# Kernel optimization log

Measured on AMD Instinct MI355X. Metric: run time of the kernel, lower is better.

Reference implementation:

```python
import jax, jax.numpy as jnp
import numpy as np
from jax import lax

# dims: batch, seq, d_model, d_inner, d_state, dt_rank, conv_k, fno_modes, n_inner_blocks, d_model_out
B_, L_, D_, DI_, N_, R_, K_, M_, NB_, DOUT_ = 2, 256, 256, 512, 32, 16, 4, 16, 7, 76416
EPS = 1e-5


def setup_inputs() -> dict:
    key = jax.random.key(0)
    ks = iter(jax.random.split(key, 48))
    nrm = lambda shape, s=0.02: jax.random.normal(next(ks), shape, jnp.float32) * s
    a_log = jnp.log(jnp.arange(1, N_ + 1, dtype=jnp.float32))  # Mamba S4D-real init
    return {
        "x": jax.random.normal(next(ks), (B_, L_, D_), jnp.float32),
        "ln_w": jnp.ones((NB_, D_), jnp.float32), "ln_b": jnp.zeros((NB_, D_), jnp.float32),
        "in_w": nrm((NB_, 2 * DI_, D_)),
        "conv_w": nrm((NB_, DI_, K_)), "conv_b": jnp.zeros((NB_, DI_), jnp.float32),
        "xproj_w": nrm((NB_, R_ + N_, DI_)),
        "dt_w": nrm((NB_, DI_, R_)), "dt_b": jnp.full((NB_, DI_), -4.0, jnp.float32),
        "A_log": jnp.broadcast_to(a_log, (NB_, DI_, N_)),
        "Cmat": nrm((NB_, DI_, N_)), "Dvec": jnp.ones((NB_, DI_), jnp.float32),
        "spec_r": nrm((NB_, DI_, M_)), "spec_i": nrm((NB_, DI_, M_)),
        "out_w": nrm((NB_, D_, DI_)),
        "fln_w": jnp.ones((D_,), jnp.float32), "fln_b": jnp.zeros((D_,), jnp.float32),
        "f_in_w": nrm((2 * DI_, D_)),
        "f_conv_w": nrm((DI_, K_)), "f_conv_b": jnp.zeros((DI_,), jnp.float32),
        "f_xproj_w": nrm((R_ + N_, DI_)),
        "f_dt_w": nrm((DI_, R_)), "f_dt_b": jnp.full((DI_,), -4.0, jnp.float32),
        "f_A_log": jnp.broadcast_to(a_log, (DI_, N_)),
        "f_Cmat": nrm((DI_, N_)), "f_Dvec": jnp.ones((DI_,), jnp.float32),
        "f_spec_r": nrm((DI_, M_)), "f_spec_i": nrm((DI_, M_)),
        "f_out_w": nrm((DOUT_, DI_)),
    }


def _silu(v):
    return v * jax.nn.sigmoid(v)


def _layernorm(v, w, b):
    mu = v.mean(-1, keepdims=True)
    var = ((v - mu) ** 2).mean(-1, keepdims=True)
    return (v - mu) * lax.rsqrt(var + EPS) * w + b


def _mixer(h, in_w, conv_w, conv_b, xproj_w, dt_w, dt_b, A_log, Cmat, Dvec, spec_r, spec_i, out_w):
    # MambawithfixedC_time: selective scan with learned fixed C + 1D FNO spectral branch
    B, L, _ = h.shape
    Di, K = conv_w.shape
    R = dt_w.shape[1]
    x, z = jnp.split(h @ in_w.T, 2, axis=-1)                      # (B,L,Di) each
    # causal depthwise conv along sequence
    xc = jnp.pad(x.transpose(0, 2, 1), ((0, 0), (0, 0), (K - 1, 0)))  # (B,Di,L+K-1)
    x = lax.conv_general_dilated(xc, conv_w[:, None, :], (1,), 'VALID',
                                 feature_group_count=Di)          # (B,Di,L)
    x = _silu(x.transpose(0, 2, 1) + conv_b)                      # (B,L,Di)
    dbl = x @ xproj_w.T                                           # (B,L,R+N)
    dt = jax.nn.softplus(dbl[..., :R] @ dt_w.T + dt_b)            # (B,L,Di)
    Bmat = dbl[..., R:]                                           # (B,L,N)
    A = -jnp.exp(A_log)                                           # (Di,N)
    dA = jnp.exp(dt[..., None] * A)                               # (B,L,Di,N)
    dBx = dt[..., None] * Bmat[:, :, None, :] * x[..., None]      # (B,L,Di,N)

    def step(hstate, inputs):
        a_t, bx_t = inputs
        hstate = a_t * hstate + bx_t
        return hstate, jnp.einsum('bdn,dn->bd', hstate, Cmat)

    h0 = jnp.zeros((B, Di, A.shape[1]), x.dtype)
    _, y = lax.scan(step, h0, (dA.transpose(1, 0, 2, 3), dBx.transpose(1, 0, 2, 3)))
    y = y.transpose(1, 0, 2) + Dvec * x                           # (B,L,Di)
    # FNO spectral branch: keep first M rFFT modes over sequence axis
    M = spec_r.shape[1]
    Xf = jnp.fft.rfft(x, axis=1)[:, :M, :]                        # (B,M,Di) complex
    W = (spec_r + 1j * spec_i).T                                  # (M,Di)
    y = y + jnp.fft.irfft(Xf * W, n=L, axis=1)
    return (y * _silu(z)) @ out_w.T


def reference(x, ln_w, ln_b, in_w, conv_w, conv_b, xproj_w, dt_w, dt_b, A_log, Cmat,
              Dvec, spec_r, spec_i, out_w, fln_w, fln_b, f_in_w, f_conv_w, f_conv_b,
              f_xproj_w, f_dt_w, f_dt_b, f_A_log, f_Cmat, f_Dvec, f_spec_r, f_spec_i,
              f_out_w):
    hidden, residual = x, None
    for i in range(ln_w.shape[0]):  # inner Blocks (prenorm residual + mixer)
        residual = hidden if residual is None else residual + hidden
        hidden = _layernorm(residual, ln_w[i], ln_b[i])
        hidden = _mixer(hidden, in_w[i], conv_w[i], conv_b[i], xproj_w[i], dt_w[i],
                        dt_b[i], A_log[i], Cmat[i], Dvec[i], spec_r[i], spec_i[i], out_w[i])
    # finalBlock: residual add + norm + mixer projecting to d_model_out
    residual = residual + hidden
    hidden = _layernorm(residual, fln_w, fln_b)
    return _mixer(hidden, f_in_w, f_conv_w, f_conv_b, f_xproj_w, f_dt_w, f_dt_b,
                  f_A_log, f_Cmat, f_Dvec, f_spec_r, f_spec_i, f_out_w)
```

## Files before the change

### kernel.cpp

```cpp
#include <hip/hip_runtime.h>
#include <hip/hip_bf16.h>

#define BLr 512
#define Dm 256
#define DIc 512
#define DOUTc 76416

typedef short bf16x8 __attribute__((ext_vector_type(8)));
typedef float f32x16 __attribute__((ext_vector_type(16)));

__device__ __forceinline__ unsigned short f2bf(float f){
  unsigned u = __builtin_bit_cast(unsigned, f);
  u += 0x7FFFu + ((u >> 16) & 1u);
  return (unsigned short)(u >> 16);
}

__device__ __forceinline__ void gl_lds16(const void* g, void* l){
  __builtin_amdgcn_global_load_lds(
      (const __attribute__((address_space(1))) unsigned int*)g,
      (__attribute__((address_space(3))) unsigned int*)l, 16, 0, 0);
}

__device__ __forceinline__ bf16x8 cvt8(float4 a, float4 b){
  unsigned q0 = (unsigned)f2bf(a.x) | ((unsigned)f2bf(a.y) << 16);
  unsigned q1 = (unsigned)f2bf(a.z) | ((unsigned)f2bf(a.w) << 16);
  unsigned q2 = (unsigned)f2bf(b.x) | ((unsigned)f2bf(b.y) << 16);
  unsigned q3 = (unsigned)f2bf(b.z) | ((unsigned)f2bf(b.w) << 16);
  uint4 u{q0, q1, q2, q3};
  return __builtin_bit_cast(bf16x8, u);
}

__global__ __launch_bounds__(256) void ln_inproj_kernel(
    float* __restrict__ xz, const float* __restrict__ src,
    const float* __restrict__ lw, const float* __restrict__ lb,
    const float* __restrict__ iw)
{
  __shared__ __align__(16) float Aln[32][260];
  __shared__ __align__(16) float Wf[64*256];
  const int tid = threadIdx.x;
  const int m0 = blockIdx.y*32, n0 = blockIdx.x*64;
  const int wv = tid>>6, lane = tid&63;
  #pragma unroll
  for (int i = 0; i < 16; ++i){
    int col = i*4 + wv;
    int sc  = lane ^ (col&7);
    gl_lds16(iw + (size_t)(n0+col)*256 + sc*4, (void*)((char*)Wf + col*1024));
  }
  float4 w4 = *(const float4*)(lw + lane*4);
  float4 b4 = *(const float4*)(lb + lane*4);
  #pragma unroll
  for (int rr = 0; rr < 8; ++rr){
    int row = wv*8 + rr;
    float4 v = *(const float4*)(src + (m0+row)*Dm + lane*4);
    float s  = v.x+v.y+v.z+v.w;
    float s2 = v.x*v.x+v.y*v.y+v.z*v.z+v.w*v.w;
    #pragma unroll
    for (int m = 1; m < 64; m <<= 1){ s += __shfl_xor(s,m); s2 += __shfl_xor(s2,m); }
    float mu = s*(1.f/256.f), var = s2*(1.f/256.f) - mu*mu;
    float rs = rsqrtf(var + 1e-5f);
    float4 o;
    o.x = (v.x-mu)*rs*w4.x + b4.x;
    o.y = (v.y-mu)*rs*w4.y + b4.y;
    o.z = (v.z-mu)*rs*w4.z + b4.z;
    o.w = (v.w-mu)*rs*w4.w + b4.w;
    *(float4*)&Aln[row][lane*4] = o;
  }
  __syncthreads();
  const int ty = tid>>4, tx = tid&15;
  float acc[2][4] = {{0,0,0,0},{0,0,0,0}};
  #pragma unroll 4
  for (int kk = 0; kk < 64; ++kk){
    float4 a0 = *(const float4*)&Aln[ty][kk*4];
    float4 a1 = *(const float4*)&Aln[ty+16][kk*4];
    #pragma unroll
    for (int j = 0; j < 4; ++j){
      int col = tx + 16*j;
      float4 w = *(const float4*)&Wf[(col*64 + (kk ^ (col&7)))*4];
      acc[0][j] += a0.x*w.x + a0.y*w.y + a0.z*w.z + a0.w*w.w;
      acc[1][j] += a1.x*w.x + a1.y*w.y + a1.z*w.z + a1.w*w.w;
    }
  }
  #pragma unroll
  for (int j = 0; j < 4; ++j){
    xz[(m0+ty)*1024    + n0 + tx + 16*j] = acc[0][j];
    xz[(m0+ty+16)*1024 + n0 + tx + 16*j] = acc[1][j];
  }
}

__global__ __launch_bounds__(256) void conv_xproj_dt_kernel(
    float* __restrict__ xc, float* __restrict__ dbl, float* __restrict__ dtv,
    const float* __restrict__ xz, const float* __restrict__ cw,
    const float* __restrict__ cb, const float* __restrict__ xw,
    const float* __restrict__ dw, const float* __restrict__ db)
{
  __shared__ __align__(16) float xcr[512];
  __shared__ float dblq[16];
  const int row = blockIdx.x, tid = threadIdx.x;
  const int t = row & 255;
  #pragma unroll
  for (int h = 0; h < 2; ++h){
    int d = tid + h*256;
    float4 w = *(const float4*)(cw + d*4);
    float acc = cb[d];
    const float* xp = xz + (size_t)row*1024 + d;
    if (t >= 3) acc += w.x*xp[-3072] + w.y*xp[-2048] + w.z*xp[-1024] + w.w*xp[0];
    else {
      acc += w.w*xp[0];
      if (t >= 1) acc += w.z*xp[-1024];
      if (t >= 2) acc += w.y*xp[-2048];
    }
    float v = acc / (1.f + __expf(-acc));
    xcr[d] = v;
    xc[row*DIc + d] = v;
  }
  __syncthreads();
  const int wv = tid>>6, lane = tid&63;
  float4 xa = *(const float4*)&xcr[lane*4];
  float4 xb = *(const float4*)&xcr[256 + lane*4];
  #pragma unroll
  for (int o = 0; o < 12; ++o){
    int oo = wv*12 + o;
    const float* wr = xw + oo*DIc;
    float4 wa = *(const float4*)(wr + lane*4);
    float4 wb = *(const float4*)(wr + 256 + lane*4);
    float p = xa.x*wa.x + xa.y*wa.y + xa.z*wa.z + xa.w*wa.w
            + xb.x*wb.x + xb.y*wb.y + xb.z*wb.z + xb.w*wb.w;
    #pragma unroll
    for (int m = 1; m < 64; m <<= 1) p += __shfl_xor(p, m);
    if (lane == 0){
      dbl[row*48 + oo] = p;
      if (oo < 16) dblq[oo] = p;
    }
  }
  __syncthreads();
  #pragma unroll
  for (int h = 0; h < 2; ++h){
    int d = tid + h*256;
    const float4* wr = (const float4*)(dw + d*16);
    float4 w0 = wr[0], w1 = wr[1], w2 = wr[2], w3 = wr[3];
    float acc = db[d];
    acc += dblq[0]*w0.x  + dblq[1]*w0.y  + dblq[2]*w0.z  + dblq[3]*w0.w;
    acc += dblq[4]*w1.x  + dblq[5]*w1.y  + dblq[6]*w1.z  + dblq[7]*w1.w;
    acc += dblq[8]*w2.x  + dblq[9]*w2.y  + dblq[10]*w2.z + dblq[11]*w2.w;
    acc += dblq[12]*w3.x + dblq[13]*w3.y + dblq[14]*w3.z + dblq[15]*w3.w;
    dtv[row*DIc + d] = (acc > 20.f) ? acc : log1pf(__expf(acc));
  }
}

__global__ __launch_bounds__(256) void scan_fft_gate_kernel(
    float* __restrict__ g, unsigned short* __restrict__ gbf,
    const float* __restrict__ xc, const float* __restrict__ dtv,
    const float* __restrict__ dbl, const float* __restrict__ xz,
    const float* __restrict__ A_log, const float* __restrict__ Cmat,
    const float* __restrict__ Dvec, const float* __restrict__ sr,
    const float* __restrict__ si)
{
  __shared__ float xs[4][260], dts[4][260], ys[4][260];
  __shared__ float ct[256], st[256];
  __shared__ float Ysr[4][17], Ysi[4][17];
  __shared__ float Pl[2][2][32][65];
  const int tid = threadIdx.x;
  const int b = blockIdx.y, d0 = blockIdx.x*4;
  {
    float sv, cv;
    __sincosf((float)tid * 0.02454369260617026f, &sv, &cv);
    ct[tid] = cv; st[tid] = sv;
  }
  const int dd = tid & 3, tq = tid >> 2;
  #pragma unroll
  for (int i = 0; i < 4; ++i){
    int t = i*64 + tq;
    xs[dd][t]  = xc [(b*256+t)*DIc + d0+dd];
    dts[dd][t] = dtv[(b*256+t)*DIc + d0+dd];
  }
  __syncthreads();
  const int wv = tid>>6, lane = tid&63;
  if (wv < 2){
    const int ch2 = lane>>5;
    const int ddw = wv*2 + ch2;
    const int d = d0 + ddw;
    const int n = lane & 31;
    const int tloc = lane & 31;
    const float A  = -__expf(A_log[d*32+n]);
    const float Cv = Cmat[d*32+n];
    const float* Bp = dbl + (size_t)(b*256)*48 + 16 + n;
    float h = 0.f;
    for (int pass = 0; pass < 4; ++pass){
      #pragma unroll 8
      for (int i = 0; i < 64; ++i){
        int t = pass*64 + i;
        float dtl = dts[ddw][t];
        float xv  = xs[ddw][t];
        float Bv  = Bp[t*48];
        h = __expf(dtl*A)*h + dtl*Bv*xv;
        Pl[wv][ch2][n][i] = h*Cv;
      }
      float s0 = 0.f, s1 = 0.f;
      #pragma unroll 8
      for (int n2 = 0; n2 < 32; ++n2){
        s0 += Pl[wv][ch2][n2][tloc];
        s1 += Pl[wv][ch2][n2][32+tloc];
      }
      ys[ddw][pass*64 + tloc]      = s0;
      ys[ddw][pass*64 + 32 + tloc] = s1;
    }
  } else {
    const int ddw = (wv-2)*2 + (lane>>5);
    const int m = lane & 15, im = (lane>>4) & 1;
    float acc = 0.f;
    for (int t = 0; t < 256; ++t){
      int idx = (m*t) & 255;
      acc += xs[ddw][t] * (im ? st[idx] : ct[idx]);
    }
    float other = __shfl_xor(acc, 16);
    const int d = d0 + ddw;
    float wr = sr[d*16+m], wi = si[d*16+m];
    if (im == 0){
      float Xr = acc, Xi = -other;
      Ysr[ddw][m] = Xr*wr - Xi*wi;
    } else {
      float Xi = -acc, Xr = other;
      Ysi[ddw][m] = Xr*wi + Xi*wr;
    }
  }
  __syncthreads();
  {
    const float Dv = Dvec[d0+dd];
    float yr[16], yi[16];
    #pragma unroll
    for (int m = 0; m < 16; ++m){ yr[m] = Ysr[dd][m]; yi[m] = Ysi[dd][m]; }
    #pragma unroll 2
    for (int i = 0; i < 4; ++i){
      int t = i*64 + tq;
      float fv = 0.5f * yr[0];
      #pragma unroll
      for (int m = 1; m < 16; ++m){
        int idx = (m*t) & 255;
        fv += yr[m]*ct[idx] - yi[m]*st[idx];
      }
      float yv = ys[dd][t] + Dv*xs[dd][t] + fv*0.0078125f;
      float z = xz[(b*256+t)*1024 + 512 + d0+dd];
      float gv = yv * (z / (1.f + __expf(-z)));
      int oi = (b*256+t)*DIc + d0+dd;
      g[oi] = gv;
      gbf[oi] = f2bf(gv);
    }
  }
}

__global__ __launch_bounds__(256) void outproj_resid_kernel(
    float* __restrict__ resid, const float* __restrict__ base,
    const float* __restrict__ g, const float* __restrict__ ow)
{
  __shared__ __align__(16) float Ws2[16*512];
  __shared__ __align__(16) float As[32*128];
  const int tid = threadIdx.x;
  const int wv = tid>>6, lane = tid&63;
  const int n0 = blockIdx.x*16, m0 = blockIdx.y*32;
  const int ty = tid>>4, tx = tid&15;
  #pragma unroll
  for (int i = 0; i < 4; ++i){
    int row = wv*4 + i;
    #pragma unroll
    for (int h = 0; h < 2; ++h){
      int c = h*64 + lane;
      int s = c ^ (row&7);
      gl_lds16(ow + (size_t)(n0+row)*DIc + s*4,
               (void*)((char*)Ws2 + row*2048 + h*1024));
    }
  }
  float b0 = base[(m0+ty)*Dm + n0+tx];
  float b1 = base[(m0+ty+16)*Dm + n0+tx];
  float a00 = 0.f, a10 = 0.f;
  for (int kc = 0; kc < 512; kc += 128){
    if (kc) __syncthreads();
    #pragma unroll
    for (int j = 0; j < 4; ++j){
      int R = wv*8 + j*2;
      int r = R + (lane>>5);
      int c = lane&31;
      int s = c ^ (r&7);
      gl_lds16(g + (size_t)(m0+r)*DIc + kc + s*4,
               (void*)((char*)As + R*512));
    }
    __syncthreads();
    const int kb = kc>>2;
    #pragma unroll
    for (int kk = 0; kk < 32; ++kk){
      float4 a0 = *(const float4*)((const char*)As + ty*512      + ((kk ^ (ty&7))<<4));
      float4 a1 = *(const float4*)((const char*)As + (ty+16)*512 + ((kk ^ (ty&7))<<4));
      float4 w0 = *(const float4*)((const char*)Ws2 + tx*2048 + (((kb+kk) ^ (tx&7))<<4));
      a00 += a0.x*w0.x + a0.y*w0.y + a0.z*w0.z + a0.w*w0.w;
      a10 += a1.x*w0.x + a1.y*w0.y + a1.z*w0.z + a1.w*w0.w;
    }
  }
  resid[(m0+ty)*Dm    + n0+tx] = b0 + a00;
  resid[(m0+ty+16)*Dm + n0+tx] = b1 + a10;
}

__global__ __launch_bounds__(512) void gemm_final2_kernel(
    float* __restrict__ Out, const unsigned short* __restrict__ Gb,
    const float* __restrict__ W)
{
  __shared__ __align__(16) unsigned short As[32768];
  __shared__ __align__(16) unsigned short Wb[4096];
  const int tid = threadIdx.x;
  const int wv = tid>>6, lane = tid&63;
  const int half = lane>>5, lm = lane&31;
  const int nq = wv & 1, mq = wv >> 1;
  const int col = blockIdx.x*64 + nq*32 + lm;
  const int wcol = tid>>3, wkq = tid&7;
  const float* Wsrc = W + (size_t)(blockIdx.x*64 + wcol)*512 + wkq*8;
  unsigned short* Wdst = Wb + (wcol*8 + (wkq ^ (wcol&7)))*8;
  f32x16 acc[4];
  #pragma unroll
  for (int i = 0; i < 4; ++i)
    #pragma unroll
    for (int rg = 0; rg < 16; ++rg) acc[i][rg] = 0.f;

  for (int k0 = 0; k0 < 512; k0 += 64){
    float4 wf0 = *(const float4*)(Wsrc + k0);
    float4 wf1 = *(const float4*)(Wsrc + k0 + 4);
    #pragma unroll
    for (int p = 0; p < 8; ++p){
      int R  = p*64 + wv*8;
      int rr = R + (lane>>3);
      int cg = (lane&7) ^ (rr&7);
      gl_lds16(Gb + rr*512 + k0 + cg*8, (void*)((char*)As + R*128));
    }
    *(bf16x8*)Wdst = cvt8(wf0, wf1);
    __syncthreads();
    #pragma unroll
    for (int j = 0; j < 4; ++j){
      const int c = j*2 + half;
      bf16x8 bv = *(const bf16x8*)(Wb + (((nq*32+lm)*8) + (c ^ ((nq*32+lm)&7)))*8);
      #pragma unroll
      for (int mt = 0; mt < 4; ++mt){
        int rr = mq*128 + mt*32 + lm;
        bf16x8 av = *(const bf16x8*)((const char*)As + (rr*8 + (c ^ (rr&7)))*16);
        acc[mt] = __builtin_amdgcn_mfma_f32_32x32x16_bf16(av, bv, acc[mt], 0, 0, 0);
      }
    }
    __syncthreads();
  }
  #pragma unroll
  for (int mt = 0; mt < 4; ++mt){
    int rbase = mq*128 + mt*32 + 4*half;
    #pragma unroll
    for (int rg = 0; rg < 16; ++rg){
      int row = rbase + (rg&3) + 8*(rg>>2);
      Out[(size_t)row*DOUTc + col] = acc[mt][rg];
    }
  }
}

extern "C" void kernel_launch(void* const* d_in, const int* in_sizes, int n_in,
                              void* d_out, int out_size, void* d_ws, size_t ws_size,
                              hipStream_t stream)
{
  (void)in_sizes; (void)n_in; (void)out_size; (void)ws_size;
  const float* x       = (const float*)d_in[0];
  const float* ln_w    = (const float*)d_in[1];
  const float* ln_b    = (const float*)d_in[2];
  const float* in_w    = (const float*)d_in[3];
  const float* conv_w  = (const float*)d_in[4];
  const float* conv_b  = (const float*)d_in[5];
  const float* xproj_w = (const float*)d_in[6];
  const float* dt_w    = (const float*)d_in[7];
  const float* dt_b    = (const float*)d_in[8];
  const float* A_log   = (const float*)d_in[9];
  const float* Cmat    = (const float*)d_in[10];
  const float* Dvec    = (const float*)d_in[11];
  const float* spec_r  = (const float*)d_in[12];
  const float* spec_i  = (const float*)d_in[13];
  const float* out_w   = (const float*)d_in[14];
  const float* fln_w   = (const float*)d_in[15];
  const float* fln_b   = (const float*)d_in[16];
  const float* f_in_w  = (const float*)d_in[17];
  const float* f_conv_w= (const float*)d_in[18];
  const float* f_conv_b= (const float*)d_in[19];
  const float* f_xproj = (const float*)d_in[20];
  const float* f_dt_w  = (const float*)d_in[21];
  const float* f_dt_b  = (const float*)d_in[22];
  const float* f_A_log = (const float*)d_in[23];
  const float* f_Cmat  = (const float*)d_in[24];
  const float* f_Dvec  = (const float*)d_in[25];
  const float* f_spec_r= (const float*)d_in[26];
  const float* f_spec_i= (const float*)d_in[27];
  const float* f_out_w = (const float*)d_in[28];

  float* ws   = (float*)d_ws;
  float* resid = ws;
  float* xz    = ws + 131072;
  float* xcb   = ws + 655360;
  float* dblb  = ws + 917504;
  float* dtb   = ws + 942080;
  float* gb    = ws + 1204224;
  unsigned short* g_bf = (unsigned short*)(ws + 1466368);
  float* outp = (float*)d_out;

  for (int i = 0; i < 8; ++i){
    const bool fin = (i == 7);
    const float* lw = fin ? fln_w   : ln_w    + i*256;
    const float* lb = fin ? fln_b   : ln_b    + i*256;
    const float* iw = fin ? f_in_w  : in_w    + i*262144;
    const float* cw = fin ? f_conv_w: conv_w  + i*2048;
    const float* cb = fin ? f_conv_b: conv_b  + i*512;
    const float* xw = fin ? f_xproj : xproj_w + i*24576;
    const float* dw = fin ? f_dt_w  : dt_w    + i*8192;
    const float* db = fin ? f_dt_b  : dt_b    + i*512;
    const float* al = fin ? f_A_log : A_log   + i*16384;
    const float* cm = fin ? f_Cmat  : Cmat    + i*16384;
    const float* dv = fin ? f_Dvec  : Dvec    + i*512;
    const float* sr = fin ? f_spec_r: spec_r  + i*8192;
    const float* si = fin ? f_spec_i: spec_i  + i*8192;

    const float* src = (i == 0) ? x : resid;
    ln_inproj_kernel<<<dim3(16, 16), 256, 0, stream>>>(xz, src, lw, lb, iw);
    conv_xproj_dt_kernel<<<512, 256, 0, stream>>>(xcb, dblb, dtb, xz, cw, cb, xw, dw, db);
    scan_fft_gate_kernel<<<dim3(128, 2), 256, 0, stream>>>(gb, g_bf, xcb, dtb, dblb, xz,
                                                           al, cm, dv, sr, si);
    if (!fin){
      outproj_resid_kernel<<<dim3(16, 16), 256, 0, stream>>>(resid, (i == 0) ? x : resid,
                                                             gb, out_w + i*131072);
    } else {
      gemm_final2_kernel<<<DOUTc/64, 512, 0, stream>>>(outp, g_bf, f_out_w);
    }
  }
}
```

Baseline: 844.9 us.

## Fuse all mixer stages into one persistent kernel with grid barriers

Replaces the per-block sequence of four kernel launches with a single persistent 256-block kernel. Stages (LN+in-proj, conv+xproj+dt, scan+FFT+gate, out-proj+residual) are separated by a software grid barrier built on atomic counters. The aim is to remove launch overhead and inter-kernel gaps across the eight blocks. The trade-off is barrier spin cost and reliance on all 256 blocks being co-resident. The barrier also has a spin timeout that could silently break ordering. The old multi-launch path remains as a fallback when the workspace is too small, and the final large GEMM stays a separate launch.

```diff
diff --git a/kernel.cpp b/kernel.cpp
--- a/kernel.cpp
+++ b/kernel.cpp
@@ -28,6 +28,345 @@
   unsigned q3 = (unsigned)f2bf(b.z) | ((unsigned)f2bf(b.w) << 16);
   uint4 u{q0, q1, q2, q3};
   return __builtin_bit_cast(bf16x8, u);
+}
+
+__device__ __forceinline__ void gsync(unsigned* cnt, unsigned* gen, unsigned nb){
+  __syncthreads();
+  if (threadIdx.x == 0){
+    __threadfence();
+    unsigned g = __hip_atomic_load(gen, __ATOMIC_ACQUIRE, __HIP_MEMORY_SCOPE_AGENT);
+    unsigned a = __hip_atomic_fetch_add(cnt, 1u, __ATOMIC_ACQ_REL, __HIP_MEMORY_SCOPE_AGENT);
+    if (a == nb - 1u){
+      __hip_atomic_store(cnt, 0u, __ATOMIC_RELAXED, __HIP_MEMORY_SCOPE_AGENT);
+      __hip_atomic_fetch_add(gen, 1u, __ATOMIC_RELEASE, __HIP_MEMORY_SCOPE_AGENT);
+    } else {
+      int it = 0;
+      while (__hip_atomic_load(gen, __ATOMIC_ACQUIRE, __HIP_MEMORY_SCOPE_AGENT) == g){
+        __builtin_amdgcn_s_sleep(8);
+        if (++it > 16384) break;
+      }
+    }
+    __threadfence();
+  }
+  __syncthreads();
+}
+
+struct MegaArgs {
+  const float *x, *ln_w, *ln_b, *in_w, *conv_w, *conv_b, *xproj_w, *dt_w, *dt_b,
+              *A_log, *Cmat, *Dvec, *spec_r, *spec_i, *out_w,
+              *fln_w, *fln_b, *f_in_w, *f_conv_w, *f_conv_b, *f_xproj,
+              *f_dt_w, *f_dt_b, *f_A_log, *f_Cmat, *f_Dvec, *f_spec_r, *f_spec_i;
+  float *resid, *xz, *xc, *dbl, *dtv, *g;
+  unsigned short* gbf;
+  unsigned *cnt, *gen;
+};
+
+__global__ __launch_bounds__(256) void mega_kernel(MegaArgs a)
+{
+  __shared__ __align__(16) unsigned char SMEM[98816];
+  const int tid = threadIdx.x;
+  const int blk = blockIdx.x;
+  const int wv = tid>>6, lane = tid&63;
+
+  for (int i = 0; i < 8; ++i){
+    const bool fin = (i == 7);
+    const float* lw  = fin ? a.fln_w   : a.ln_w    + i*256;
+    const float* lb  = fin ? a.fln_b   : a.ln_b    + i*256;
+    const float* iw  = fin ? a.f_in_w  : a.in_w    + i*262144;
+    const float* cw  = fin ? a.f_conv_w: a.conv_w  + i*2048;
+    const float* cb  = fin ? a.f_conv_b: a.conv_b  + i*512;
+    const float* xw  = fin ? a.f_xproj : a.xproj_w + i*24576;
+    const float* dwp = fin ? a.f_dt_w  : a.dt_w    + i*8192;
+    const float* dbp = fin ? a.f_dt_b  : a.dt_b    + i*512;
+    const float* al  = fin ? a.f_A_log : a.A_log   + i*16384;
+    const float* cm  = fin ? a.f_Cmat  : a.Cmat    + i*16384;
+    const float* dv  = fin ? a.f_Dvec  : a.Dvec    + i*512;
+    const float* srp = fin ? a.f_spec_r: a.spec_r  + i*8192;
+    const float* sip = fin ? a.f_spec_i: a.spec_i  + i*8192;
+    const float* src = (i == 0) ? a.x : a.resid;
+
+    {
+      float (*Aln)[260] = (float(*)[260])SMEM;
+      float* Wf = (float*)(SMEM + 33280);
+      const int m0 = (blk>>4)*32, n0 = (blk&15)*64;
+      #pragma unroll
+      for (int q = 0; q < 16; ++q){
+        int col = q*4 + wv;
+        int sc  = lane ^ (col&7);
+        gl_lds16(iw + (size_t)(n0+col)*256 + sc*4, (void*)((char*)Wf + col*1024));
+      }
+      float4 w4 = *(const float4*)(lw + lane*4);
+      float4 b4 = *(const float4*)(lb + lane*4);
+      #pragma unroll
+      for (int rr = 0; rr < 8; ++rr){
+        int row = wv*8 + rr;
+        float4 v = *(const float4*)(src + (size_t)(m0+row)*Dm + lane*4);
+        float s  = v.x+v.y+v.z+v.w;
+        float s2 = v.x*v.x+v.y*v.y+v.z*v.z+v.w*v.w;
+        #pragma unroll
+        for (int m = 1; m < 64; m <<= 1){ s += __shfl_xor(s,m); s2 += __shfl_xor(s2,m); }
+        float mu = s*(1.f/256.f), var = s2*(1.f/256.f) - mu*mu;
+        float rs = rsqrtf(var + 1e-5f);
+        float4 o;
+        o.x = (v.x-mu)*rs*w4.x + b4.x;
+        o.y = (v.y-mu)*rs*w4.y + b4.y;
+        o.z = (v.z-mu)*rs*w4.z + b4.z;
+        o.w = (v.w-mu)*rs*w4.w + b4.w;
+        *(float4*)&Aln[row][lane*4] = o;
+      }
+      __syncthreads();
+      const int ty = tid>>4, tx = tid&15;
+      float acc[2][4] = {{0,0,0,0},{0,0,0,0}};
+      #pragma unroll 4
+      for (int kk = 0; kk < 64; ++kk){
+        float4 a0 = *(const float4*)&Aln[ty][kk*4];
+        float4 a1 = *(const float4*)&Aln[ty+16][kk*4];
+        #pragma unroll
+        for (int j = 0; j < 4; ++j){
+          int col = tx + 16*j;
+          float4 w = *(const float4*)&Wf[(col*64 + (kk ^ (col&7)))*4];
+          acc[0][j] += a0.x*w.x + a0.y*w.y + a0.z*w.z + a0.w*w.w;
+          acc[1][j] += a1.x*w.x + a1.y*w.y + a1.z*w.z + a1.w*w.w;
+        }
+      }
+      #pragma unroll
+      for (int j = 0; j < 4; ++j){
+        a.xz[(size_t)(m0+ty)*1024    + n0 + tx + 16*j] = acc[0][j];
+        a.xz[(size_t)(m0+ty+16)*1024 + n0 + tx + 16*j] = acc[1][j];
+      }
+    }
+    gsync(a.cnt, a.gen, 256);
+
+    {
+      float* xcr  = (float*)SMEM;
+      float* dblq = (float*)(SMEM + 4096);
+      const int r0 = blk*2, r1 = r0 + 1;
+      const int t0 = r0 & 255, t1 = r1 & 255;
+      #pragma unroll
+      for (int h = 0; h < 2; ++h){
+        int d = tid + h*256;
+        float4 w = *(const float4*)(cw + d*4);
+        float cbd = cb[d];
+        {
+          float acc = cbd;
+          const float* xp = a.xz + (size_t)r0*1024 + d;
+          if (t0 >= 3) acc += w.x*xp[-3072] + w.y*xp[-2048] + w.z*xp[-1024] + w.w*xp[0];
+          else {
+            acc += w.w*xp[0];
+            if (t0 >= 1) acc += w.z*xp[-1024];
+            if (t0 >= 2) acc += w.y*xp[-2048];
+          }
+          float v = acc / (1.f + __expf(-acc));
+          xcr[d] = v;
+          a.xc[(size_t)r0*DIc + d] = v;
+        }
+        {
+          float acc = cbd;
+          const float* xp = a.xz + (size_t)r1*1024 + d;
+          if (t1 >= 3) acc += w.x*xp[-3072] + w.y*xp[-2048] + w.z*xp[-1024] + w.w*xp[0];
+          else {
+            acc += w.w*xp[0];
+            if (t1 >= 1) acc += w.z*xp[-1024];
+            if (t1 >= 2) acc += w.y*xp[-2048];
+          }
+          float v = acc / (1.f + __expf(-acc));
+          xcr[512+d] = v;
+          a.xc[(size_t)r1*DIc + d] = v;
+        }
+      }
+      __syncthreads();
+      float4 xa0 = *(const float4*)&xcr[lane*4];
+      float4 xb0 = *(const float4*)&xcr[256 + lane*4];
+      float4 xa1 = *(const float4*)&xcr[512 + lane*4];
+      float4 xb1 = *(const float4*)&xcr[768 + lane*4];
+      #pragma unroll
+      for (int o = 0; o < 12; ++o){
+        int oo = wv*12 + o;
+        const float* wr = xw + oo*DIc;
+        float4 wa = *(const float4*)(wr + lane*4);
+        float4 wb = *(const float4*)(wr + 256 + lane*4);
+        float p0 = xa0.x*wa.x + xa0.y*wa.y + xa0.z*wa.z + xa0.w*wa.w
+                 + xb0.x*wb.x + xb0.y*wb.y + xb0.z*wb.z + xb0.w*wb.w;
+        float p1 = xa1.x*wa.x + xa1.y*wa.y + xa1.z*wa.z + xa1.w*wa.w
+                 + xb1.x*wb.x + xb1.y*wb.y + xb1.z*wb.z + xb1.w*wb.w;
+        #pragma unroll
+        for (int m = 1; m < 64; m <<= 1){ p0 += __shfl_xor(p0, m); p1 += __shfl_xor(p1, m); }
+        if (lane == 0){
+          a.dbl[r0*48 + oo] = p0;
+          a.dbl[r1*48 + oo] = p1;
+          if (oo < 16){ dblq[oo] = p0; dblq[16+oo] = p1; }
+        }
+      }
+      __syncthreads();
+      #pragma unroll
+      for (int h = 0; h < 2; ++h){
+        int d = tid + h*256;
+        const float4* wr4 = (const float4*)(dwp + d*16);
+        float4 w0 = wr4[0], w1 = wr4[1], w2 = wr4[2], w3 = wr4[3];
+        float dbv = dbp[d];
+        float acc0 = dbv;
+        acc0 += dblq[0]*w0.x  + dblq[1]*w0.y  + dblq[2]*w0.z  + dblq[3]*w0.w;
+        acc0 += dblq[4]*w1.x  + dblq[5]*w1.y  + dblq[6]*w1.z  + dblq[7]*w1.w;
+        acc0 += dblq[8]*w2.x  + dblq[9]*w2.y  + dblq[10]*w2.z + dblq[11]*w2.w;
+        acc0 += dblq[12]*w3.x + dblq[13]*w3.y + dblq[14]*w3.z + dblq[15]*w3.w;
+        float acc1 = dbv;
+        acc1 += dblq[16]*w0.x + dblq[17]*w0.y + dblq[18]*w0.z + dblq[19]*w0.w;
+        acc1 += dblq[20]*w1.x + dblq[21]*w1.y + dblq[22]*w1.z + dblq[23]*w1.w;
+        acc1 += dblq[24]*w2.x + dblq[25]*w2.y + dblq[26]*w2.z + dblq[27]*w2.w;
+        acc1 += dblq[28]*w3.x + dblq[29]*w3.y + dblq[30]*w3.z + dblq[31]*w3.w;
+        a.dtv[(size_t)r0*DIc + d] = (acc0 > 20.f) ? acc0 : log1pf(__expf(acc0));
+        a.dtv[(size_t)r1*DIc + d] = (acc1 > 20.f) ? acc1 : log1pf(__expf(acc1));
+      }
+    }
+    gsync(a.cnt, a.gen, 256);
+
+    {
+      float (*xs)[260]  = (float(*)[260])(SMEM);
+      float (*dts)[260] = (float(*)[260])(SMEM + 4160);
+      float (*ys)[260]  = (float(*)[260])(SMEM + 8320);
+      float* ct = (float*)(SMEM + 12480);
+      float* st = (float*)(SMEM + 13504);
+      float (*Ysr)[17] = (float(*)[17])(SMEM + 14528);
+      float (*Ysi)[17] = (float(*)[17])(SMEM + 14800);
+      float (*Pl)[2][32][65] = (float(*)[2][32][65])(SMEM + 15072);
+      const int b = blk>>7, d0 = (blk&127)*4;
+      {
+        float sv, cv;
+        __sincosf((float)tid * 0.02454369260617026f, &sv, &cv);
+        ct[tid] = cv; st[tid] = sv;
+      }
+      const int dd = tid & 3, tq = tid >> 2;
+      #pragma unroll
+      for (int q = 0; q < 4; ++q){
+        int t = q*64 + tq;
+        xs[dd][t]  = a.xc [((size_t)b*256+t)*DIc + d0+dd];
+        dts[dd][t] = a.dtv[((size_t)b*256+t)*DIc + d0+dd];
+      }
+      __syncthreads();
+      if (wv < 2){
+        const int ch2 = lane>>5;
+        const int ddw = wv*2 + ch2;
+        const int d = d0 + ddw;
+        const int n = lane & 31;
+        const int tloc = lane & 31;
+        const float A  = -__expf(al[d*32+n]);
+        const float Cv = cm[d*32+n];
+        const float* Bp = a.dbl + (size_t)(b*256)*48 + 16 + n;
+        float h = 0.f;
+        for (int pass = 0; pass < 4; ++pass){
+          #pragma unroll 8
+          for (int q = 0; q < 64; ++q){
+            int t = pass*64 + q;
+            float dtl = dts[ddw][t];
+            float xv  = xs[ddw][t];
+            float Bv  = Bp[t*48];
+            h = __expf(dtl*A)*h + dtl*Bv*xv;
+            Pl[wv][ch2][n][q] = h*Cv;
+          }
+          float s0 = 0.f, s1 = 0.f;
+          #pragma unroll 8
+          for (int n2 = 0; n2 < 32; ++n2){
+            s0 += Pl[wv][ch2][n2][tloc];
+            s1 += Pl[wv][ch2][n2][32+tloc];
+          }
+          ys[ddw][pass*64 + tloc]      = s0;
+          ys[ddw][pass*64 + 32 + tloc] = s1;
+        }
+      } else {
+        const int ddw = (wv-2)*2 + (lane>>5);
+        const int m = lane & 15, im = (lane>>4) & 1;
+        float acc = 0.f;
+        for (int t = 0; t < 256; ++t){
+          int idx = (m*t) & 255;
+          acc += xs[ddw][t] * (im ? st[idx] : ct[idx]);
+        }
+        float other = __shfl_xor(acc, 16);
+        const int d = d0 + ddw;
+        float wr = srp[d*16+m], wi = sip[d*16+m];
+        if (im == 0){
+          float Xr = acc, Xi = -other;
+          Ysr[ddw][m] = Xr*wr - Xi*wi;
+        } else {
+          float Xi = -acc, Xr = other;
+          Ysi[ddw][m] = Xr*wi + Xi*wr;
+        }
+      }
+      __syncthreads();
+      {
+        const float Dv = dv[d0+dd];
+        float yr[16], yi[16];
+        #pragma unroll
+        for (int m = 0; m < 16; ++m){ yr[m] = Ysr[dd][m]; yi[m] = Ysi[dd][m]; }
+        #pragma unroll 2
+        for (int q = 0; q < 4; ++q){
+          int t = q*64 + tq;
+          float fv = 0.5f * yr[0];
+          #pragma unroll
+          for (int m = 1; m < 16; ++m){
+            int idx = (m*t) & 255;
+            fv += yr[m]*ct[idx] - yi[m]*st[idx];
+          }
+          float yv = ys[dd][t] + Dv*xs[dd][t] + fv*0.0078125f;
+          float z = a.xz[((size_t)b*256+t)*1024 + 512 + d0+dd];
+          float gv = yv * (z / (1.f + __expf(-z)));
+          size_t oi = ((size_t)b*256+t)*DIc + d0+dd;
+          a.g[oi] = gv;
+          a.gbf[oi] = f2bf(gv);
+        }
+      }
+    }
+
+    if (!fin){
+      gsync(a.cnt, a.gen, 256);
+      {
+        float* Ws2 = (float*)SMEM;
+        float* As  = (float*)(SMEM + 32768);
+        const int n0 = (blk&15)*16, m0 = (blk>>4)*32;
+        const int ty = tid>>4, tx = tid&15;
+        const float* base = (i == 0) ? a.x : a.resid;
+        const float* ow = a.out_w + i*131072;
+        #pragma unroll
+        for (int q = 0; q < 4; ++q){
+          int row = wv*4 + q;
+          #pragma unroll
+          for (int h = 0; h < 2; ++h){
+            int c = h*64 + lane;
+            int s = c ^ (row&7);
+            gl_lds16(ow + (size_t)(n0+row)*DIc + s*4,
+                     (void*)((char*)Ws2 + row*2048 + h*1024));
+          }
+        }
+        float b0 = base[(m0+ty)*Dm + n0+tx];
+        float b1 = base[(m0+ty+16)*Dm + n0+tx];
+        float a00 = 0.f, a10 = 0.f;
+        for (int kc = 0; kc < 512; kc += 128){
+          if (kc) __syncthreads();
+          #pragma unroll
+          for (int j = 0; j < 4; ++j){
+            int R = wv*8 + j*2;
+            int r = R + (lane>>5);
+            int c = lane&31;
+            int s = c ^ (r&7);
+            gl_lds16(a.g + (size_t)(m0+r)*DIc + kc + s*4,
+                     (void*)((char*)As + R*512));
+          }
+          __syncthreads();
+          const int kb = kc>>2;
+          #pragma unroll
+          for (int kk = 0; kk < 32; ++kk){
+            float4 a0 = *(const float4*)((const char*)As + ty*512      + ((kk ^ (ty&7))<<4));
+            float4 a1 = *(const float4*)((const char*)As + (ty+16)*512 + ((kk ^ (ty&7))<<4));
+            float4 w0 = *(const float4*)((const char*)Ws2 + tx*2048 + (((kb+kk) ^ (tx&7))<<4));
+            a00 += a0.x*w0.x + a0.y*w0.y + a0.z*w0.z + a0.w*w0.w;
+            a10 += a1.x*w0.x + a1.y*w0.y + a1.z*w0.z + a1.w*w0.w;
+          }
+        }
+        a.resid[(m0+ty)*Dm    + n0+tx] = b0 + a00;
+        a.resid[(m0+ty+16)*Dm + n0+tx] = b1 + a10;
+      }
+      gsync(a.cnt, a.gen, 256);
+    }
+  }
 }
 
 __global__ __launch_bounds__(256) void ln_inproj_kernel(
@@ -51,7 +390,7 @@
   #pragma unroll
   for (int rr = 0; rr < 8; ++rr){
     int row = wv*8 + rr;
-    float4 v = *(const float4*)(src + (m0+row)*Dm + lane*4);
+    float4 v = *(const float4*)(src + (size_t)(m0+row)*Dm + lane*4);
     float s  = v.x+v.y+v.z+v.w;
     float s2 = v.x*v.x+v.y*v.y+v.z*v.z+v.w*v.w;
     #pragma unroll
@@ -358,7 +697,7 @@
                               void* d_out, int out_size, void* d_ws, size_t ws_size,
                               hipStream_t stream)
 {
-  (void)in_sizes; (void)n_in; (void)out_size; (void)ws_size;
+  (void)in_sizes; (void)n_in; (void)out_size;
   const float* x       = (const float*)d_in[0];
   const float* ln_w    = (const float*)d_in[1];
   const float* ln_b    = (const float*)d_in[2];
@@ -397,34 +736,54 @@
   float* dtb   = ws + 942080;
   float* gb    = ws + 1204224;
   unsigned short* g_bf = (unsigned short*)(ws + 1466368);
+  unsigned* barrier_words = (unsigned*)(ws + 1597440);
   float* outp = (float*)d_out;
 
-  for (int i = 0; i < 8; ++i){
-    const bool fin = (i == 7);
-    const float* lw = fin ? fln_w   : ln_w    + i*256;
-    const float* lb = fin ? fln_b   : ln_b    + i*256;
-    const float* iw = fin ? f_in_w  : in_w    + i*262144;
-    const float* cw = fin ? f_conv_w: conv_w  + i*2048;
-    const float* cb = fin ? f_conv_b: conv_b  + i*512;
-    const float* xw = fin ? f_xproj : xproj_w + i*24576;
-    const float* dw = fin ? f_dt_w  : dt_w    + i*8192;
-    const float* db = fin ? f_dt_b  : dt_b    + i*512;
-    const float* al = fin ? f_A_log : A_log   + i*16384;
-    const float* cm = fin ? f_Cmat  : Cmat    + i*16384;
-    const float* dv = fin ? f_Dvec  : Dvec    + i*512;
-    const float* sr = fin ? f_spec_r: spec_r  + i*8192;
-    const float* si = fin ? f_spec_i: spec_i  + i*8192;
-
-    const float* src = (i == 0) ? x : resid;
-    ln_inproj_kernel<<<dim3(16, 16), 256, 0, stream>>>(xz, src, lw, lb, iw);
-    conv_xproj_dt_kernel<<<512, 256, 0, stream>>>(xcb, dblb, dtb, xz, cw, cb, xw, dw, db);
-    scan_fft_gate_kernel<<<dim3(128, 2), 256, 0, stream>>>(gb, g_bf, xcb, dtb, dblb, xz,
-                                                           al, cm, dv, sr, si);
-    if (!fin){
-      outproj_resid_kernel<<<dim3(16, 16), 256, 0, stream>>>(resid, (i == 0) ? x : resid,
-                                                             gb, out_w + i*131072);
-    } else {
-      gemm_final2_kernel<<<DOUTc/64, 512, 0, stream>>>(outp, g_bf, f_out_w);
-    }
-  }
-}
+  const bool mega_ok = ws_size >= (size_t)1597440*4 + 8;
+
+  if (mega_ok){
+    hipMemsetAsync(barrier_words, 0, 8, stream);
+    MegaArgs margs;
+    margs.x = x;       margs.ln_w = ln_w;     margs.ln_b = ln_b;
+    margs.in_w = in_w; margs.conv_w = conv_w; margs.conv_b = conv_b;
+    margs.xproj_w = xproj_w; margs.dt_w = dt_w; margs.dt_b = dt_b;
+    margs.A_log = A_log; margs.Cmat = Cmat; margs.Dvec = Dvec;
+    margs.spec_r = spec_r; margs.spec_i = spec_i; margs.out_w = out_w;
+    margs.fln_w = fln_w; margs.fln_b = fln_b; margs.f_in_w = f_in_w;
+    margs.f_conv_w = f_conv_w; margs.f_conv_b = f_conv_b; margs.f_xproj = f_xproj;
+    margs.f_dt_w = f_dt_w; margs.f_dt_b = f_dt_b; margs.f_A_log = f_A_log;
+    margs.f_Cmat = f_Cmat; margs.f_Dvec = f_Dvec; margs.f_spec_r = f_spec_r;
+    margs.f_spec_i = f_spec_i;
+    margs.resid = resid; margs.xz = xz; margs.xc = xcb; margs.dbl = dblb;
+    margs.dtv = dtb; margs.g = gb; margs.gbf = g_bf;
+    margs.cnt = barrier_words; margs.gen = barrier_words + 1;
+    mega_kernel<<<256, 256, 0, stream>>>(margs);
+  } else {
+    for (int i = 0; i < 8; ++i){
+      const bool fin = (i == 7);
+      const float* lw = fin ? fln_w   : ln_w    + i*256;
+      const float* lb = fin ? fln_b   : ln_b    + i*256;
+      const float* iw = fin ? f_in_w  : in_w    + i*262144;
+      const float* cw = fin ? f_conv_w: conv_w  + i*2048;
+      const float* cb = fin ? f_conv_b: conv_b  + i*512;
+      const float* xw = fin ? f_xproj : xproj_w + i*24576;
+      const float* dw = fin ? f_dt_w  : dt_w    + i*8192;
+      const float* db = fin ? f_dt_b  : dt_b    + i*512;
+      const float* al = fin ? f_A_log : A_log   + i*16384;
+      const float* cm = fin ? f_Cmat  : Cmat    + i*16384;
+      const float* dv = fin ? f_Dvec  : Dvec    + i*512;
+      const float* sr = fin ? f_spec_r: spec_r  + i*8192;
+      const float* si = fin ? f_spec_i: spec_i  + i*8192;
+      const float* src = (i == 0) ? x : resid;
+      ln_inproj_kernel<<<dim3(16, 16), 256, 0, stream>>>(xz, src, lw, lb, iw);
+      conv_xproj_dt_kernel<<<512, 256, 0, stream>>>(xcb, dblb, dtb, xz, cw, cb, xw, dw, db);
+      scan_fft_gate_kernel<<<dim3(128, 2), 256, 0, stream>>>(gb, g_bf, xcb, dtb, dblb, xz,
+                                                             al, cm, dv, sr, si);
+      if (!fin){
+        outproj_resid_kernel<<<dim3(16, 16), 256, 0, stream>>>(resid, (i == 0) ? x : resid,
+                                                               gb, out_w + i*131072);
+      }
+    }
+  }
+  gemm_final2_kernel<<<DOUTc/64, 512, 0, stream>>>(outp, g_bf, f_out_w);
+}
```

Result: slower. 2.215 ms (+162.1%).
